# Kernel optimization log

Measured on AMD Instinct MI355X. Metric: run time of the kernel, lower is better.

Reference implementation:

```python
import jax, jax.numpy as jnp
import numpy as np

B, C1, C2, K, S, P, D, HDIM, BINS = 4, 32, 64, 3, 1, 1, 1, 64, 16
H = W = 96

def _unfold(x):
    # torch F.unfold: (B, C*k*k, L) with channel-major (c, kh, kw) ordering,
    # which matches conv_general_dilated_patches' output feature ordering.
    p = jax.lax.conv_general_dilated_patches(
        x, filter_shape=(K, K), window_strides=(S, S),
        padding=((P, P), (P, P)), rhs_dilation=(D, D))  # (B, C*k*k, Ho, Wo)
    b, ckk, ho, wo = p.shape
    return p.reshape(b, ckk, ho * wo), ho, wo

def _patch_stats(patches):
    # patches: (B, Ckk, L); stop-gradient stats [mu, sigma, gamma, kappa, entropy]
    b, ckk, L = patches.shape
    mu = patches.mean(axis=1, keepdims=True)
    diff = patches - mu
    var = (diff * diff).mean(axis=1, keepdims=True)
    sigma = jnp.sqrt(var + 1e-6)
    z = diff / (sigma + 1e-6)
    gamma = (z ** 3).mean(axis=1, keepdims=True)
    kappa = (z ** 4).mean(axis=1, keepdims=True) - 3.0
    p_min = patches.min(axis=1, keepdims=True)
    p_max = patches.max(axis=1, keepdims=True)
    p_norm = (patches - p_min) / (p_max - p_min + 1e-6)
    bin_idx = jnp.clip((p_norm * (BINS - 1)).astype(jnp.int32), 0, BINS - 1)
    # histogram via flat scatter-add: counts[b, bin, l]
    b_ix = jnp.arange(b, dtype=jnp.int32)[:, None, None]
    l_ix = jnp.arange(L, dtype=jnp.int32)[None, None, :]
    flat = ((b_ix * BINS + bin_idx) * L + l_ix).ravel()
    counts = jnp.zeros(b * BINS * L, dtype=patches.dtype).at[flat].add(1.0)
    counts = counts.reshape(b, BINS, L)
    prob = counts / (ckk + 1e-6)
    entropy = -(prob * jnp.log(prob + 1e-9)).sum(axis=1, keepdims=True)
    stats = jnp.concatenate([mu, sigma, gamma, kappa, entropy], axis=1)  # (B,5,L)
    return jax.lax.stop_gradient(stats)

def setup_inputs() -> dict:
    key = jax.random.key(0)
    ks = jax.random.split(key, 8)
    x = jax.random.normal(ks[0], (B, C1, H, W), dtype=jnp.float32)
    fc1_w = jax.random.normal(ks[1], (HDIM, 5), dtype=jnp.float32) / np.sqrt(5.0)
    fc1_b = jax.random.normal(ks[2], (HDIM,), dtype=jnp.float32) * 0.01
    alpha_w = jax.random.normal(ks[3], (C2, HDIM), dtype=jnp.float32) * 0.01
    alpha_b = jnp.ones((C2,), dtype=jnp.float32)
    phi_w = jax.random.normal(ks[4], (C1 * K * K, HDIM), dtype=jnp.float32) * 0.01
    phi_b = jnp.zeros((C1 * K * K,), dtype=jnp.float32)
    bn_gamma = jnp.ones((C2,), dtype=jnp.float32)
    bn_beta = jnp.zeros((C2,), dtype=jnp.float32)
    bn_mean = jax.random.normal(ks[5], (C2,), dtype=jnp.float32) * 0.1
    bn_var = jax.random.uniform(ks[6], (C2,), dtype=jnp.float32, minval=0.5, maxval=1.5)
    return {"x": x, "fc1_w": fc1_w, "fc1_b": fc1_b, "alpha_w": alpha_w,
            "alpha_b": alpha_b, "phi_w": phi_w, "phi_b": phi_b,
            "bn_gamma": bn_gamma, "bn_beta": bn_beta,
            "bn_mean": bn_mean, "bn_var": bn_var}

def reference(x, fc1_w, fc1_b, alpha_w, alpha_b, phi_w, phi_b,
              bn_gamma, bn_beta, bn_mean, bn_var):
    patches, ho, wo = _unfold(x)           # (B, C1*K*K, L)
    b, ckk, L = patches.shape
    stats = _patch_stats(patches)          # (B, 5, L), stop-grad
    s = stats.transpose(0, 2, 1).reshape(b * L, 5)
    h = jax.nn.relu(s @ fc1_w.T + fc1_b)                 # (B*L, HDIM)
    alpha = (h @ alpha_w.T + alpha_b).reshape(b, L, C2)  # (B, L, C2)
    phi = (h @ phi_w.T + phi_b).reshape(b, L, ckk)       # (B, L, Ckk)
    # kernel = alpha[:,None] * phi[None,:]; out = kernel @ patch
    # == alpha * (phi . patch), computed without materializing kernels
    proj = jnp.einsum('blj,bjl->bl', phi, patches)       # (B, L)
    out = alpha * proj[:, :, None]                       # (B, L, C2)
    out = out.transpose(0, 2, 1).reshape(b, C2, ho, wo)
    # BatchNorm2d (eval: running stats) + SiLU
    inv = bn_gamma / jnp.sqrt(bn_var + 1e-5)
    y = (out - bn_mean[None, :, None, None]) * inv[None, :, None, None] \
        + bn_beta[None, :, None, None]
    return jax.nn.silu(y)
```

## Files before the change

kernel.cpp:

```cpp
#include <hip/hip_runtime.h>

#define FLT_MAX_ 3.402823466e+38f

constexpr int HW   = 9216;
constexpr int AOFF = 4608;

using bf16x8 = __attribute__((ext_vector_type(8))) short;
using f32x4  = __attribute__((ext_vector_type(4))) float;
using u32x4  = __attribute__((ext_vector_type(4))) unsigned int;

__device__ inline unsigned cvtpk_bf16(float a, float b) {
    unsigned r;
    asm("v_cvt_pk_bf16_f32 %0, %1, %2" : "=v"(r) : "v"(a), "v"(b));
    return r;
}
__device__ inline void split2(float p0, float p1, unsigned &h, unsigned &l) {
    h = cvtpk_bf16(p0, p1);
    const float h0 = __builtin_bit_cast(float, h << 16);
    const float h1 = __builtin_bit_cast(float, h & 0xFFFF0000u);
    l = cvtpk_bf16(p0 - h0, p1 - h1);
}

__global__ __launch_bounds__(256)
void prep_w(const float* __restrict__ phi_w, const float* __restrict__ alpha_w,
            u32x4* __restrict__ wsq) {
    const int kb   = blockIdx.x;
    const int n    = threadIdx.x >> 6;
    const int lane = threadIdx.x & 63;
    const int lg   = lane >> 4, kk = lane & 15;
    if (kb < 9) {
        float p[8];
        #pragma unroll
        for (int jj = 0; jj < 8; ++jj) {
            const int ch = lg * 8 + jj;
            p[jj] = phi_w[(ch * 9 + kb) * 64 + n * 16 + kk];
        }
        unsigned h0,h1,h2,h3, l0,l1,l2,l3;
        split2(p[0],p[1],h0,l0); split2(p[2],p[3],h1,l1);
        split2(p[4],p[5],h2,l2); split2(p[6],p[7],h3,l3);
        wsq[(kb * 4 + n) * 64 + lane]        = u32x4{h0,h1,h2,h3};
        wsq[2304 + (kb * 4 + n) * 64 + lane] = u32x4{l0,l1,l2,l3};
    } else {
        #pragma unroll
        for (int kblk = 0; kblk < 2; ++kblk) {
            float p[8];
            #pragma unroll
            for (int jj = 0; jj < 8; ++jj) {
                const int k = kblk * 32 + lg * 8 + jj;
                p[jj] = alpha_w[(n * 16 + kk) * 64 + k];
            }
            unsigned h0,h1,h2,h3, l0,l1,l2,l3;
            split2(p[0],p[1],h0,l0); split2(p[2],p[3],h1,l1);
            split2(p[4],p[5],h2,l2); split2(p[6],p[7],h3,l3);
            wsq[AOFF + (kblk * 4 + n) * 64 + lane]       = u32x4{h0,h1,h2,h3};
            wsq[AOFF + 512 + (kblk * 4 + n) * 64 + lane] = u32x4{l0,l1,l2,l3};
        }
    }
}

__global__ __launch_bounds__(256, 6)
void sac_fused(const float* __restrict__ x,
               const float* __restrict__ fc1_w, const float* __restrict__ fc1_b,
               const float* __restrict__ alpha_b,
               const float* __restrict__ phi_b,
               const float* __restrict__ bn_g, const float* __restrict__ bn_b,
               const float* __restrict__ bn_m, const float* __restrict__ bn_v,
               const u32x4* __restrict__ wsq,
               float* __restrict__ out)
{
    __shared__ float    h_lds[32 * 65];
    __shared__ unsigned cnts[16 * 33];
    __shared__ float    phib[32];
    __shared__ float    redP[64];

    const int tid  = threadIdx.x;
    const int lane = tid & 63;
    const int w    = __builtin_amdgcn_readfirstlane(tid >> 6);
    const int g    = blockIdx.x;
    const int b    = g / 288;
    const int rem  = g - b * 288;
    const int y0   = rem / 3;
    const int x0   = (rem - y0 * 3) * 32;

    const int p8  = lane & 7;
    const int cg  = lane >> 3;
    const int pos = w * 8 + p8;
    const int col = x0 + pos;

    const float* __restrict__ xb = x + (size_t)b * 32 * HW;

    float pv[36];
    float s1 = 0.f, s2 = 0.f, s3 = 0.f, s4 = 0.f;
    float mn = FLT_MAX_, mx = -FLT_MAX_, pj = 0.f;
    {
        const float* __restrict__ xc = xb + (size_t)(cg * 4) * HW;
        #pragma unroll
        for (int cc = 0; cc < 4; ++cc) {
            const float* __restrict__ xcc = xc + (size_t)cc * HW;
            const float* __restrict__ pbp = phi_b + (cg * 4 + cc) * 9;
            #pragma unroll
            for (int dy = 0; dy < 3; ++dy) {
                const int y    = y0 + dy - 1;
                const bool yok = (unsigned)y < 96u;
                #pragma unroll
                for (int dx = 0; dx < 3; ++dx) {
                    const int xx  = col + dx - 1;
                    const bool ok = yok && ((unsigned)xx < 96u);
                    const float p = ok ? xcc[y * 96 + xx] : 0.f;
                    pv[cc * 9 + dy * 3 + dx] = p;
                    const float pp = p * p;
                    s1 += p;
                    s2 = fmaf(p, p, s2);
                    s3 = fmaf(pp, p, s3);
                    s4 = fmaf(pp, pp, s4);
                    mn = fminf(mn, p);
                    mx = fmaxf(mx, p);
                    pj = fmaf(p, pbp[dy * 3 + dx], pj);
                }
            }
        }
    }
    #pragma unroll
    for (int msk = 8; msk < 64; msk <<= 1) {
        s1 += __shfl_xor(s1, msk);
        s2 += __shfl_xor(s2, msk);
        s3 += __shfl_xor(s3, msk);
        s4 += __shfl_xor(s4, msk);
        mn = fminf(mn, __shfl_xor(mn, msk));
        mx = fmaxf(mx, __shfl_xor(mx, msk));
        pj += __shfl_xor(pj, msk);
    }
    if (cg == 0) phib[pos] = pj;

    const float mu   = s1 * (1.0f / 288.0f);
    const float rng  = (mx - mn) + 1e-6f;
    const float invr = 1.0f / rng;

    cnts[(cg * 2 + 0) * 33 + pos] = 0u;
    cnts[(cg * 2 + 1) * 33 + pos] = 0u;
    asm volatile("s_waitcnt lgkmcnt(0)" ::: "memory");
    #pragma unroll
    for (int i = 0; i < 36; ++i) {
        const float pn = (pv[i] - mn) * invr;
        int bi = (int)(pn * 15.0f);
        bi = bi < 0 ? 0 : (bi > 15 ? 15 : bi);
        atomicAdd(&cnts[bi * 33 + pos], 1u);
    }
    asm volatile("s_waitcnt lgkmcnt(0)" ::: "memory");
    float ent = 0.f;
    #pragma unroll
    for (int e = 0; e < 2; ++e) {
        const float prob = (float)cnts[(cg * 2 + e) * 33 + pos] * (1.0f / 288.0f);
        ent -= prob * __logf(prob + 1e-9f);
    }
    #pragma unroll
    for (int msk = 8; msk < 64; msk <<= 1) ent += __shfl_xor(ent, msk);

    {
        const float e2  = s2 * (1.0f / 288.0f);
        const float e3  = s3 * (1.0f / 288.0f);
        const float e4  = s4 * (1.0f / 288.0f);
        const float mu2 = mu * mu;
        const float var = fmaxf(e2 - mu2, 0.f);
        const float m3  = e3 - 3.f * mu * e2 + 2.f * mu * mu2;
        const float m4  = e4 - 4.f * mu * e3 + 6.f * mu2 * e2 - 3.f * mu2 * mu2;
        const float sig = sqrtf(var + 1e-6f);
        const float inv = 1.0f / (sig + 1e-6f);
        const float inv2 = inv * inv;
        const float gam = m3 * (inv2 * inv);
        const float kap = m4 * (inv2 * inv2) - 3.0f;
        #pragma unroll
        for (int kk = 0; kk < 8; ++kk) {
            const int k = cg * 8 + kk;
            float acc = fc1_b[k];
            acc = fmaf(mu,  fc1_w[k * 5 + 0], acc);
            acc = fmaf(sig, fc1_w[k * 5 + 1], acc);
            acc = fmaf(gam, fc1_w[k * 5 + 2], acc);
            acc = fmaf(kap, fc1_w[k * 5 + 3], acc);
            acc = fmaf(ent, fc1_w[k * 5 + 4], acc);
            h_lds[pos * 65 + k] = fmaxf(acc, 0.f);
        }
    }
    __syncthreads();

    const int m  = w >> 1;
    const int np = (w & 1) * 2;
    const int lg = lane >> 4;

    {
        const int posa = m * 16 + (lane & 15);
        const int cola = x0 + posa;
        const float* __restrict__ xg8 = xb + (size_t)(lg * 8) * HW;

        f32x4 acc0 = {0.f, 0.f, 0.f, 0.f};
        f32x4 acc1 = {0.f, 0.f, 0.f, 0.f};

        #pragma unroll
        for (int tap = 0; tap < 9; ++tap) {
            const int dy = tap / 3, dx = tap % 3;
            const u32x4 bh0 = wsq[(tap * 4 + np) * 64 + lane];
            const u32x4 bh1 = wsq[(tap * 4 + np + 1) * 64 + lane];
            const u32x4 bl0 = wsq[2304 + (tap * 4 + np) * 64 + lane];
            const u32x4 bl1 = wsq[2304 + (tap * 4 + np + 1) * 64 + lane];

            const int ya = y0 + dy - 1, xa = cola + dx - 1;
            const bool ok = ((unsigned)ya < 96u) && ((unsigned)xa < 96u);
            const int off = ya * 96 + xa;
            const float p0 = ok ? xg8[0 * HW + off] : 0.f;
            const float p1 = ok ? xg8[1 * HW + off] : 0.f;
            const float p2 = ok ? xg8[2 * HW + off] : 0.f;
            const float p3 = ok ? xg8[3 * HW + off] : 0.f;
            const float p4 = ok ? xg8[4 * HW + off] : 0.f;
            const float p5 = ok ? xg8[5 * HW + off] : 0.f;
            const float p6 = ok ? xg8[6 * HW + off] : 0.f;
            const float p7 = ok ? xg8[7 * HW + off] : 0.f;
            unsigned ah0,ah1,ah2,ah3, al0,al1,al2,al3;
            split2(p0,p1,ah0,al0); split2(p2,p3,ah1,al1);
            split2(p4,p5,ah2,al2); split2(p6,p7,ah3,al3);
            const bf16x8 Ah  = __builtin_bit_cast(bf16x8, u32x4{ah0,ah1,ah2,ah3});
            const bf16x8 Al  = __builtin_bit_cast(bf16x8, u32x4{al0,al1,al2,al3});
            const bf16x8 Bh0 = __builtin_bit_cast(bf16x8, bh0);
            const bf16x8 Bl0 = __builtin_bit_cast(bf16x8, bl0);
            const bf16x8 Bh1 = __builtin_bit_cast(bf16x8, bh1);
            const bf16x8 Bl1 = __builtin_bit_cast(bf16x8, bl1);

            acc0 = __builtin_amdgcn_mfma_f32_16x16x32_bf16(Ah, Bh0, acc0, 0, 0, 0);
            acc0 = __builtin_amdgcn_mfma_f32_16x16x32_bf16(Ah, Bl0, acc0, 0, 0, 0);
            acc0 = __builtin_amdgcn_mfma_f32_16x16x32_bf16(Al, Bh0, acc0, 0, 0, 0);
            acc1 = __builtin_amdgcn_mfma_f32_16x16x32_bf16(Ah, Bh1, acc1, 0, 0, 0);
            acc1 = __builtin_amdgcn_mfma_f32_16x16x32_bf16(Ah, Bl1, acc1, 0, 0, 0);
            acc1 = __builtin_amdgcn_mfma_f32_16x16x32_bf16(Al, Bh1, acc1, 0, 0, 0);
        }

        const int k0 = np * 16 + (lane & 15);
        const int k1 = k0 + 16;
        const int pbr = (m * 16 + lg * 4) * 65;
        float pr0 = acc0[0] * h_lds[pbr + 0 * 65 + k0] + acc1[0] * h_lds[pbr + 0 * 65 + k1];
        float pr1 = acc0[1] * h_lds[pbr + 1 * 65 + k0] + acc1[1] * h_lds[pbr + 1 * 65 + k1];
        float pr2 = acc0[2] * h_lds[pbr + 2 * 65 + k0] + acc1[2] * h_lds[pbr + 2 * 65 + k1];
        float pr3 = acc0[3] * h_lds[pbr + 3 * 65 + k0] + acc1[3] * h_lds[pbr + 3 * 65 + k1];
        #pragma unroll
        for (int msk = 1; msk < 16; msk <<= 1) {
            pr0 += __shfl_xor(pr0, msk);
            pr1 += __shfl_xor(pr1, msk);
            pr2 += __shfl_xor(pr2, msk);
            pr3 += __shfl_xor(pr3, msk);
        }
        if ((lane & 15) == 0) {
            const int pb = m * 16 + lg * 4;
            redP[(pb + 0) * 2 + (w & 1)] = pr0;
            redP[(pb + 1) * 2 + (w & 1)] = pr1;
            redP[(pb + 2) * 2 + (w & 1)] = pr2;
            redP[(pb + 3) * 2 + (w & 1)] = pr3;
        }
    }
    __syncthreads();

    const int pb4 = m * 16 + lg * 4;
    const float pj0 = redP[(pb4 + 0) * 2] + redP[(pb4 + 0) * 2 + 1] + phib[pb4 + 0];
    const float pj1 = redP[(pb4 + 1) * 2] + redP[(pb4 + 1) * 2 + 1] + phib[pb4 + 1];
    const float pj2 = redP[(pb4 + 2) * 2] + redP[(pb4 + 2) * 2 + 1] + phib[pb4 + 2];
    const float pj3 = redP[(pb4 + 3) * 2] + redP[(pb4 + 3) * 2 + 1] + phib[pb4 + 3];

    f32x4 ac0 = {0.f, 0.f, 0.f, 0.f};
    f32x4 ac1 = {0.f, 0.f, 0.f, 0.f};
    #pragma unroll
    for (int kblk = 0; kblk < 2; ++kblk) {
        const float* hp = &h_lds[(m * 16 + (lane & 15)) * 65 + kblk * 32 + lg * 8];
        const float h0 = hp[0], h1 = hp[1], h2 = hp[2], h3 = hp[3];
        const float h4 = hp[4], h5 = hp[5], h6 = hp[6], h7 = hp[7];
        unsigned ah0,ah1,ah2,ah3, al0,al1,al2,al3;
        split2(h0,h1,ah0,al0); split2(h2,h3,ah1,al1);
        split2(h4,h5,ah2,al2); split2(h6,h7,ah3,al3);
        const bf16x8 Ah = __builtin_bit_cast(bf16x8, u32x4{ah0,ah1,ah2,ah3});
        const bf16x8 Al = __builtin_bit_cast(bf16x8, u32x4{al0,al1,al2,al3});
        const u32x4 bh0 = wsq[AOFF + (kblk * 4 + np) * 64 + lane];
        const u32x4 bh1 = wsq[AOFF + (kblk * 4 + np + 1) * 64 + lane];
        const u32x4 bl0 = wsq[AOFF + 512 + (kblk * 4 + np) * 64 + lane];
        const u32x4 bl1 = wsq[AOFF + 512 + (kblk * 4 + np + 1) * 64 + lane];
        const bf16x8 Bh0 = __builtin_bit_cast(bf16x8, bh0);
        const bf16x8 Bl0 = __builtin_bit_cast(bf16x8, bl0);
        const bf16x8 Bh1 = __builtin_bit_cast(bf16x8, bh1);
        const bf16x8 Bl1 = __builtin_bit_cast(bf16x8, bl1);
        ac0 = __builtin_amdgcn_mfma_f32_16x16x32_bf16(Ah, Bh0, ac0, 0, 0, 0);
        ac0 = __builtin_amdgcn_mfma_f32_16x16x32_bf16(Ah, Bl0, ac0, 0, 0, 0);
        ac0 = __builtin_amdgcn_mfma_f32_16x16x32_bf16(Al, Bh0, ac0, 0, 0, 0);
        ac1 = __builtin_amdgcn_mfma_f32_16x16x32_bf16(Ah, Bh1, ac1, 0, 0, 0);
        ac1 = __builtin_amdgcn_mfma_f32_16x16x32_bf16(Ah, Bl1, ac1, 0, 0, 0);
        ac1 = __builtin_amdgcn_mfma_f32_16x16x32_bf16(Al, Bh1, ac1, 0, 0, 0);
    }

    const int c0 = np * 16 + (lane & 15);
    const size_t obase = (size_t)(b * 64) * HW + (size_t)y0 * 96 + x0 + m * 16 + lg * 4;
    {
        const int ch     = c0;
        const float ab_  = alpha_b[ch];
        const float binv = bn_g[ch] * rsqrtf(bn_v[ch] + 1e-5f);
        const float bm_  = bn_m[ch], bb_ = bn_b[ch];
        const float o0 = (ac0[0] + ab_) * pj0, o1 = (ac0[1] + ab_) * pj1;
        const float o2 = (ac0[2] + ab_) * pj2, o3 = (ac0[3] + ab_) * pj3;
        const float y0v = (o0 - bm_) * binv + bb_;
        const float y1v = (o1 - bm_) * binv + bb_;
        const float y2v = (o2 - bm_) * binv + bb_;
        const float y3v = (o3 - bm_) * binv + bb_;
        f32x4 sv;
        sv[0] = __fdividef(y0v, 1.0f + __expf(-y0v));
        sv[1] = __fdividef(y1v, 1.0f + __expf(-y1v));
        sv[2] = __fdividef(y2v, 1.0f + __expf(-y2v));
        sv[3] = __fdividef(y3v, 1.0f + __expf(-y3v));
        *(f32x4*)&out[obase + (size_t)ch * HW] = sv;
    }
    {
        const int ch     = c0 + 16;
        const float ab_  = alpha_b[ch];
        const float binv = bn_g[ch] * rsqrtf(bn_v[ch] + 1e-5f);
        const float bm_  = bn_m[ch], bb_ = bn_b[ch];
        const float o0 = (ac1[0] + ab_) * pj0, o1 = (ac1[1] + ab_) * pj1;
        const float o2 = (ac1[2] + ab_) * pj2, o3 = (ac1[3] + ab_) * pj3;
        const float y0v = (o0 - bm_) * binv + bb_;
        const float y1v = (o1 - bm_) * binv + bb_;
        const float y2v = (o2 - bm_) * binv + bb_;
        const float y3v = (o3 - bm_) * binv + bb_;
        f32x4 sv;
        sv[0] = __fdividef(y0v, 1.0f + __expf(-y0v));
        sv[1] = __fdividef(y1v, 1.0f + __expf(-y1v));
        sv[2] = __fdividef(y2v, 1.0f + __expf(-y2v));
        sv[3] = __fdividef(y3v, 1.0f + __expf(-y3v));
        *(f32x4*)&out[obase + (size_t)ch * HW] = sv;
    }
}

extern "C" void kernel_launch(void* const* d_in, const int* in_sizes, int n_in,
                              void* d_out, int out_size, void* d_ws, size_t ws_size,
                              hipStream_t stream) {
    const float* x   = (const float*)d_in[0];
    const float* f1w = (const float*)d_in[1];
    const float* f1b = (const float*)d_in[2];
    const float* aw  = (const float*)d_in[3];
    const float* ab  = (const float*)d_in[4];
    const float* pw  = (const float*)d_in[5];
    const float* pb  = (const float*)d_in[6];
    const float* bg  = (const float*)d_in[7];
    const float* bb  = (const float*)d_in[8];
    const float* bm  = (const float*)d_in[9];
    const float* bv  = (const float*)d_in[10];

    u32x4* wsq = (u32x4*)d_ws;

    prep_w<<<dim3(10), dim3(256), 0, stream>>>(pw, aw, wsq);
    sac_fused<<<dim3(1152), dim3(256), 0, stream>>>(
        x, f1w, f1b, ab, pb, bg, bb, bm, bv, wsq, (float*)d_out);
}
```

Before: 35.70 us.

## Stage input halo tile in LDS as packed bf16 hi/lo pairs

Each block now loads its 32-channel, 3-row by 35-column input halo once into shared memory. Each value is stored pre-split into bf16 high and low halves packed in one word. The stats pass, histogram pass and MFMA projection pass all read from this tile instead of issuing repeated strided global loads with bounds checks, and the MFMA operands are built with byte permutes. The histogram counters are replicated four ways per position to reduce atomic contention, and the weight fragments for the next tap are prefetched one tap ahead. In exchange it uses about 13 KB more shared memory, drops the occupancy hint from launch bounds, and reconstructs values from bf16 hi+lo, which may not be bit-exact.

New measurement: 32.51 us. -8.9%, faster.

```diff
diff --git a/kernel.cpp b/kernel.cpp
--- a/kernel.cpp
+++ b/kernel.cpp
@@ -4,6 +4,8 @@
 
 constexpr int HW   = 9216;
 constexpr int AOFF = 4608;
+constexpr int CST  = 105;
+constexpr int XSW  = 32 * CST;
 
 using bf16x8 = __attribute__((ext_vector_type(8))) short;
 using f32x4  = __attribute__((ext_vector_type(4))) float;
@@ -58,7 +60,7 @@
     }
 }
 
-__global__ __launch_bounds__(256, 6)
+__global__ __launch_bounds__(256)
 void sac_fused(const float* __restrict__ x,
                const float* __restrict__ fc1_w, const float* __restrict__ fc1_b,
                const float* __restrict__ alpha_b,
@@ -68,8 +70,9 @@
                const u32x4* __restrict__ wsq,
                float* __restrict__ out)
 {
+    __shared__ unsigned xs[XSW];
     __shared__ float    h_lds[32 * 65];
-    __shared__ unsigned cnts[16 * 33];
+    __shared__ unsigned cnts[16 * 132];
     __shared__ float    phib[32];
     __shared__ float    redP[64];
 
@@ -82,32 +85,50 @@
     const int y0   = rem / 3;
     const int x0   = (rem - y0 * 3) * 32;
 
-    const int p8  = lane & 7;
-    const int cg  = lane >> 3;
-    const int pos = w * 8 + p8;
-    const int col = x0 + pos;
+    const int p8   = lane & 7;
+    const int cg   = lane >> 3;
+    const int pos  = w * 8 + p8;
+    const int cgh  = cg >> 1;
+    const int mycol = pos * 4 + cgh;
 
     const float* __restrict__ xb = x + (size_t)b * 32 * HW;
 
-    float pv[36];
+    #pragma unroll
+    for (int i = 0; i < 14; ++i) {
+        const int idx = tid + i * 256;
+        if (idx < XSW) {
+            const int ch = idx / CST;
+            const int rm = idx - ch * CST;
+            const int r2 = rm / 35;
+            const int c2 = rm - r2 * 35;
+            const int y  = y0 + r2 - 1;
+            const int xg = x0 + c2 - 1;
+            float p = 0.f;
+            if ((unsigned)y < 96u && (unsigned)xg < 96u)
+                p = xb[ch * HW + y * 96 + xg];
+            const unsigned t  = cvtpk_bf16(p, p);
+            const float    hf = __builtin_bit_cast(float, t << 16);
+            xs[idx] = cvtpk_bf16(p - hf, p);
+        }
+    }
+    #pragma unroll
+    for (int bi = 0; bi < 16; ++bi) cnts[bi * 132 + mycol] = 0u;
+    __syncthreads();
+
     float s1 = 0.f, s2 = 0.f, s3 = 0.f, s4 = 0.f;
     float mn = FLT_MAX_, mx = -FLT_MAX_, pj = 0.f;
     {
-        const float* __restrict__ xc = xb + (size_t)(cg * 4) * HW;
-        #pragma unroll
-        for (int cc = 0; cc < 4; ++cc) {
-            const float* __restrict__ xcc = xc + (size_t)cc * HW;
-            const float* __restrict__ pbp = phi_b + (cg * 4 + cc) * 9;
+        const unsigned* __restrict__ xsc = xs + (cg * 4) * CST;
+        #pragma unroll
+        for (int cc = 0; cc < 4; ++cc)
             #pragma unroll
-            for (int dy = 0; dy < 3; ++dy) {
-                const int y    = y0 + dy - 1;
-                const bool yok = (unsigned)y < 96u;
+            for (int dy = 0; dy < 3; ++dy)
                 #pragma unroll
                 for (int dx = 0; dx < 3; ++dx) {
-                    const int xx  = col + dx - 1;
-                    const bool ok = yok && ((unsigned)xx < 96u);
-                    const float p = ok ? xcc[y * 96 + xx] : 0.f;
-                    pv[cc * 9 + dy * 3 + dx] = p;
+                    const unsigned Wd = xsc[cc * CST + dy * 35 + pos + dx];
+                    const float hf = __builtin_bit_cast(float, Wd & 0xFFFF0000u);
+                    const float lf = __builtin_bit_cast(float, Wd << 16);
+                    const float p  = hf + lf;
                     const float pp = p * p;
                     s1 += p;
                     s2 = fmaf(p, p, s2);
@@ -115,10 +136,8 @@
                     s4 = fmaf(pp, pp, s4);
                     mn = fminf(mn, p);
                     mx = fmaxf(mx, p);
-                    pj = fmaf(p, pbp[dy * 3 + dx], pj);
+                    pj = fmaf(p, phi_b[(cg * 4 + cc) * 9 + dy * 3 + dx], pj);
                 }
-            }
-        }
     }
     #pragma unroll
     for (int msk = 8; msk < 64; msk <<= 1) {
@@ -136,21 +155,33 @@
     const float rng  = (mx - mn) + 1e-6f;
     const float invr = 1.0f / rng;
 
-    cnts[(cg * 2 + 0) * 33 + pos] = 0u;
-    cnts[(cg * 2 + 1) * 33 + pos] = 0u;
+    {
+        const unsigned* __restrict__ xsc = xs + (cg * 4) * CST;
+        #pragma unroll
+        for (int cc = 0; cc < 4; ++cc)
+            #pragma unroll
+            for (int dy = 0; dy < 3; ++dy)
+                #pragma unroll
+                for (int dx = 0; dx < 3; ++dx) {
+                    const unsigned Wd = xsc[cc * CST + dy * 35 + pos + dx];
+                    const float hf = __builtin_bit_cast(float, Wd & 0xFFFF0000u);
+                    const float lf = __builtin_bit_cast(float, Wd << 16);
+                    const float p  = hf + lf;
+                    const float pn = (p - mn) * invr;
+                    int bi = (int)(pn * 15.0f);
+                    bi = bi < 0 ? 0 : (bi > 15 ? 15 : bi);
+                    atomicAdd(&cnts[bi * 132 + mycol], 1u);
+                }
+    }
     asm volatile("s_waitcnt lgkmcnt(0)" ::: "memory");
-    #pragma unroll
-    for (int i = 0; i < 36; ++i) {
-        const float pn = (pv[i] - mn) * invr;
-        int bi = (int)(pn * 15.0f);
-        bi = bi < 0 ? 0 : (bi > 15 ? 15 : bi);
-        atomicAdd(&cnts[bi * 33 + pos], 1u);
-    }
-    asm volatile("s_waitcnt lgkmcnt(0)" ::: "memory");
+
     float ent = 0.f;
     #pragma unroll
     for (int e = 0; e < 2; ++e) {
-        const float prob = (float)cnts[(cg * 2 + e) * 33 + pos] * (1.0f / 288.0f);
+        const int bi = cg * 2 + e;
+        const unsigned cnt = cnts[bi * 132 + pos * 4 + 0] + cnts[bi * 132 + pos * 4 + 1]
+                           + cnts[bi * 132 + pos * 4 + 2] + cnts[bi * 132 + pos * 4 + 3];
+        const float prob = (float)cnt * (1.0f / 288.0f);
         ent -= prob * __logf(prob + 1e-9f);
     }
     #pragma unroll
@@ -170,8 +201,8 @@
         const float gam = m3 * (inv2 * inv);
         const float kap = m4 * (inv2 * inv2) - 3.0f;
         #pragma unroll
-        for (int kk = 0; kk < 8; ++kk) {
-            const int k = cg * 8 + kk;
+        for (int kk2 = 0; kk2 < 8; ++kk2) {
+            const int k = cg * 8 + kk2;
             float acc = fc1_b[k];
             acc = fmaf(mu,  fc1_w[k * 5 + 0], acc);
             acc = fmaf(sig, fc1_w[k * 5 + 1], acc);
@@ -186,37 +217,43 @@
     const int m  = w >> 1;
     const int np = (w & 1) * 2;
     const int lg = lane >> 4;
-
-    {
-        const int posa = m * 16 + (lane & 15);
-        const int cola = x0 + posa;
-        const float* __restrict__ xg8 = xb + (size_t)(lg * 8) * HW;
+    const int kk = lane & 15;
+
+    {
+        const int acol = m * 16 + kk;
+        const unsigned* __restrict__ xsg = xs + (lg * 8) * CST;
 
         f32x4 acc0 = {0.f, 0.f, 0.f, 0.f};
         f32x4 acc1 = {0.f, 0.f, 0.f, 0.f};
 
+        u32x4 nbh0 = wsq[(0 * 4 + np) * 64 + lane];
+        u32x4 nbh1 = wsq[(0 * 4 + np + 1) * 64 + lane];
+        u32x4 nbl0 = wsq[2304 + (0 * 4 + np) * 64 + lane];
+        u32x4 nbl1 = wsq[2304 + (0 * 4 + np + 1) * 64 + lane];
+
         #pragma unroll
         for (int tap = 0; tap < 9; ++tap) {
             const int dy = tap / 3, dx = tap % 3;
-            const u32x4 bh0 = wsq[(tap * 4 + np) * 64 + lane];
-            const u32x4 bh1 = wsq[(tap * 4 + np + 1) * 64 + lane];
-            const u32x4 bl0 = wsq[2304 + (tap * 4 + np) * 64 + lane];
-            const u32x4 bl1 = wsq[2304 + (tap * 4 + np + 1) * 64 + lane];
-
-            const int ya = y0 + dy - 1, xa = cola + dx - 1;
-            const bool ok = ((unsigned)ya < 96u) && ((unsigned)xa < 96u);
-            const int off = ya * 96 + xa;
-            const float p0 = ok ? xg8[0 * HW + off] : 0.f;
-            const float p1 = ok ? xg8[1 * HW + off] : 0.f;
-            const float p2 = ok ? xg8[2 * HW + off] : 0.f;
-            const float p3 = ok ? xg8[3 * HW + off] : 0.f;
-            const float p4 = ok ? xg8[4 * HW + off] : 0.f;
-            const float p5 = ok ? xg8[5 * HW + off] : 0.f;
-            const float p6 = ok ? xg8[6 * HW + off] : 0.f;
-            const float p7 = ok ? xg8[7 * HW + off] : 0.f;
-            unsigned ah0,ah1,ah2,ah3, al0,al1,al2,al3;
-            split2(p0,p1,ah0,al0); split2(p2,p3,ah1,al1);
-            split2(p4,p5,ah2,al2); split2(p6,p7,ah3,al3);
+            const u32x4 bh0 = nbh0, bh1 = nbh1, bl0 = nbl0, bl1 = nbl1;
+            if (tap < 8) {
+                nbh0 = wsq[((tap + 1) * 4 + np) * 64 + lane];
+                nbh1 = wsq[((tap + 1) * 4 + np + 1) * 64 + lane];
+                nbl0 = wsq[2304 + ((tap + 1) * 4 + np) * 64 + lane];
+                nbl1 = wsq[2304 + ((tap + 1) * 4 + np + 1) * 64 + lane];
+            }
+            const int abase = dy * 35 + acol + dx;
+            const unsigned W0 = xsg[0 * CST + abase], W1 = xsg[1 * CST + abase];
+            const unsigned W2 = xsg[2 * CST + abase], W3 = xsg[3 * CST + abase];
+            const unsigned W4 = xsg[4 * CST + abase], W5 = xsg[5 * CST + abase];
+            const unsigned W6 = xsg[6 * CST + abase], W7 = xsg[7 * CST + abase];
+            const unsigned ah0 = __builtin_amdgcn_perm(W1, W0, 0x07060302u);
+            const unsigned ah1 = __builtin_amdgcn_perm(W3, W2, 0x07060302u);
+            const unsigned ah2 = __builtin_amdgcn_perm(W5, W4, 0x07060302u);
+            const unsigned ah3 = __builtin_amdgcn_perm(W7, W6, 0x07060302u);
+            const unsigned al0 = __builtin_amdgcn_perm(W1, W0, 0x05040100u);
+            const unsigned al1 = __builtin_amdgcn_perm(W3, W2, 0x05040100u);
+            const unsigned al2 = __builtin_amdgcn_perm(W5, W4, 0x05040100u);
+            const unsigned al3 = __builtin_amdgcn_perm(W7, W6, 0x05040100u);
             const bf16x8 Ah  = __builtin_bit_cast(bf16x8, u32x4{ah0,ah1,ah2,ah3});
             const bf16x8 Al  = __builtin_bit_cast(bf16x8, u32x4{al0,al1,al2,al3});
             const bf16x8 Bh0 = __builtin_bit_cast(bf16x8, bh0);
@@ -232,7 +269,7 @@
             acc1 = __builtin_amdgcn_mfma_f32_16x16x32_bf16(Al, Bh1, acc1, 0, 0, 0);
         }
 
-        const int k0 = np * 16 + (lane & 15);
+        const int k0 = np * 16 + kk;
         const int k1 = k0 + 16;
         const int pbr = (m * 16 + lg * 4) * 65;
         float pr0 = acc0[0] * h_lds[pbr + 0 * 65 + k0] + acc1[0] * h_lds[pbr + 0 * 65 + k1];
@@ -246,7 +283,7 @@
             pr2 += __shfl_xor(pr2, msk);
             pr3 += __shfl_xor(pr3, msk);
         }
-        if ((lane & 15) == 0) {
+        if (kk == 0) {
             const int pb = m * 16 + lg * 4;
             redP[(pb + 0) * 2 + (w & 1)] = pr0;
             redP[(pb + 1) * 2 + (w & 1)] = pr1;
@@ -266,7 +303,7 @@
     f32x4 ac1 = {0.f, 0.f, 0.f, 0.f};
     #pragma unroll
     for (int kblk = 0; kblk < 2; ++kblk) {
-        const float* hp = &h_lds[(m * 16 + (lane & 15)) * 65 + kblk * 32 + lg * 8];
+        const float* hp = &h_lds[(m * 16 + kk) * 65 + kblk * 32 + lg * 8];
         const float h0 = hp[0], h1 = hp[1], h2 = hp[2], h3 = hp[3];
         const float h4 = hp[4], h5 = hp[5], h6 = hp[6], h7 = hp[7];
         unsigned ah0,ah1,ah2,ah3, al0,al1,al2,al3;
@@ -290,7 +327,7 @@
         ac1 = __builtin_amdgcn_mfma_f32_16x16x32_bf16(Al, Bh1, ac1, 0, 0, 0);
     }
 
-    const int c0 = np * 16 + (lane & 15);
+    const int c0 = np * 16 + kk;
     const size_t obase = (size_t)(b * 64) * HW + (size_t)y0 * 96 + x0 + m * 16 + lg * 4;
     {
         const int ch     = c0;
```
